# Kernel tuning notes

Hardware: AMD Instinct MI355X
Metric: run time of the kernel (lower is better)

Reference implementation:

```python
import jax, jax.numpy as jnp
import numpy as np

SAMPLE_SIZE = 8192
K = 8
N_SPLATS = 1_000_000
EPS = 1e-12  # keeps sqrt grad finite on zero-distance (duplicate) pairs


def setup_inputs() -> dict:
    key = jax.random.key(0)
    k1, k2, k3 = jax.random.split(key, 3)
    means = jax.random.normal(k1, (N_SPLATS, 3), dtype=jnp.float32)
    sh0 = jax.random.normal(k2, (N_SPLATS, 1, 3), dtype=jnp.float32)
    idx = jax.random.randint(k3, (SAMPLE_SIZE,), 0, N_SPLATS, dtype=jnp.int64)
    return {"means": means, "sh0": sh0, "idx": idx}


def reference(means, sh0, idx):
    sh0 = sh0.squeeze(1)                    # [N, 3]
    sm = means[idx]                         # [S, 3] sampled positions
    ss = sh0[idx]                           # [S, 3] sampled colors
    # pairwise euclidean distances (torch.cdist, p=2): [S, S]
    sq = jnp.sum(sm * sm, axis=-1)
    d2 = sq[:, None] + sq[None, :] - 2.0 * (sm @ sm.T)
    dist = jnp.sqrt(jnp.maximum(d2, EPS))
    # k+1 smallest per row; drop self (column 0)
    _, knn_idx = jax.lax.top_k(-dist, K + 1)           # [S, K+1]
    knn_idx = knn_idx[:, 1:]                           # [S, K]
    neighbors_sh0 = ss[knn_idx]                        # [S, K, 3]
    neighbor_dist = jnp.take_along_axis(dist, knn_idx, axis=1)[..., None]  # [S, K, 1]
    weight = jnp.exp(-neighbor_dist)
    diff = ss[:, None, :] - neighbors_sh0              # [S, K, 3]
    return jnp.mean(weight * diff * diff)
```

## Files before the change

### kernel.cpp

```cpp
#include <hip/hip_runtime.h>
#include <float.h>
#include <math.h>

#define NSAMPLE 8192
#define KSEL 9
#define KNN 8
#define BLK 512
#define EPS_F 1e-12f

#define ROWS_PB 8
#define NBLOCKS (NSAMPLE / ROWS_PB)
#define RPT 8
#define LANES 64
#define KQT 16
#define CHUNK 128
#define NCHUNK (1024 / CHUNK)
#define BNDI 4
#define WCAP 28
#define BP 129
#define IDX_MASK 0x1FFFu
#define VAL_MASK 0xFFFFE000u
#define PROW 73
#define SROW 145
#define SCALE (1.0f / (float)(NSAMPLE * KNN * 3))

#define SMEM_BYTES 40256
#define OFF_SCRATCH 4128
#define OFF_PARTS   8768
#define OFF_WL      32768
#define OFF_WCNT    39936
#define OFF_BND     40192
#define OFF_RED     40224

__device__ __forceinline__ unsigned umn(unsigned a, unsigned b) { return a < b ? a : b; }
__device__ __forceinline__ unsigned umx(unsigned a, unsigned b) { return a > b ? a : b; }

__device__ __forceinline__ void insert9(unsigned s[KSEL], unsigned x)
{
#pragma unroll
    for (int k = 0; k < KSEL - 1; ++k)
        s[k] = umx(s[k + 1], umn(x, s[k]));
    s[KSEL - 1] = umn(x, s[KSEL - 1]);
}

__device__ __forceinline__ unsigned pack_d2(float d2, int gidx)
{
    return (__float_as_uint(fmaxf(d2, 0.0f)) & VAL_MASK) | (unsigned)gidx;
}

__device__ __forceinline__ float sfl(float x)
{
    return __uint_as_float((unsigned)__builtin_amdgcn_readfirstlane(
        (int)__float_as_uint(x)));
}

__device__ __forceinline__ unsigned mbcnt64(unsigned long long m)
{
    return __builtin_amdgcn_mbcnt_hi((unsigned)(m >> 32),
           __builtin_amdgcn_mbcnt_lo((unsigned)(m & 0xFFFFFFFFull), 0u));
}

__device__ __forceinline__ void load_lds16(const float4* g, float4* l)
{
    __builtin_amdgcn_global_load_lds(
        (const __attribute__((address_space(1))) void*)g,
        (__attribute__((address_space(3))) void*)l, 16, 0, 0);
}

__global__ __launch_bounds__(256) void gather_k(
    const float* __restrict__ means, const float* __restrict__ sh0,
    const int* __restrict__ idx,
    float4* __restrict__ sm4, float4* __restrict__ ss4)
{
    int i = blockIdx.x * 256 + threadIdx.x;
    if (i >= NSAMPLE) return;
    int id = idx[i];
    const float* m = means + 3 * id;
    const float* s = sh0 + 3 * id;
    float mx = m[0], my = m[1], mz = m[2];
    sm4[i] = make_float4(mx, my, mz, fmaf(mx, mx, fmaf(my, my, mz * mz)));
    ss4[i] = make_float4(s[0], s[1], s[2], 0.0f);
}

#define QUAD(R, Q, CI)                                                        \
    {                                                                         \
        float v0 = fmaf(cX[(R) + 0], (Q).x, fmaf(cY[(R) + 0], (Q).y,          \
                   fmaf(cZ[(R) + 0], (Q).z, (Q).w)));                         \
        float v1 = fmaf(cX[(R) + 1], (Q).x, fmaf(cY[(R) + 1], (Q).y,          \
                   fmaf(cZ[(R) + 1], (Q).z, (Q).w)));                         \
        float v2 = fmaf(cX[(R) + 2], (Q).x, fmaf(cY[(R) + 2], (Q).y,          \
                   fmaf(cZ[(R) + 2], (Q).z, (Q).w)));                         \
        float v3 = fmaf(cX[(R) + 3], (Q).x, fmaf(cY[(R) + 3], (Q).y,          \
                   fmaf(cZ[(R) + 3], (Q).z, (Q).w)));                         \
        unsigned long long m0 = __ballot(v0 <= sb[(R) + 0]);                  \
        unsigned long long m1 = __ballot(v1 <= sb[(R) + 1]);                  \
        unsigned long long m2 = __ballot(v2 <= sb[(R) + 2]);                  \
        unsigned long long m3 = __ballot(v3 <= sb[(R) + 3]);                  \
        if (m0) {                                                             \
            unsigned pos = base[(R) + 0] + mbcnt64(m0);                       \
            if ((v0 <= sb[(R) + 0]) && pos < WCAP)                            \
                wl[(w * RPT + (R) + 0) * WCAP + pos] =                        \
                    pack_d2(v0 + cW[(R) + 0], (CI));                          \
            base[(R) + 0] += (unsigned)__popcll(m0);                          \
        }                                                                     \
        if (m1) {                                                             \
            unsigned pos = base[(R) + 1] + mbcnt64(m1);                       \
            if ((v1 <= sb[(R) + 1]) && pos < WCAP)                            \
                wl[(w * RPT + (R) + 1) * WCAP + pos] =                        \
                    pack_d2(v1 + cW[(R) + 1], (CI));                          \
            base[(R) + 1] += (unsigned)__popcll(m1);                          \
        }                                                                     \
        if (m2) {                                                             \
            unsigned pos = base[(R) + 2] + mbcnt64(m2);                       \
            if ((v2 <= sb[(R) + 2]) && pos < WCAP)                            \
                wl[(w * RPT + (R) + 2) * WCAP + pos] =                        \
                    pack_d2(v2 + cW[(R) + 2], (CI));                          \
            base[(R) + 2] += (unsigned)__popcll(m2);                          \
        }                                                                     \
        if (m3) {                                                             \
            unsigned pos = base[(R) + 3] + mbcnt64(m3);                       \
            if ((v3 <= sb[(R) + 3]) && pos < WCAP)                            \
                wl[(w * RPT + (R) + 3) * WCAP + pos] =                        \
                    pack_d2(v3 + cW[(R) + 3], (CI));                          \
            base[(R) + 3] += (unsigned)__popcll(m3);                          \
        }                                                                     \
    }

__global__ __launch_bounds__(BLK, 8) void main_k(
    const float4* __restrict__ sm4, const float4* __restrict__ ss4,
    float* __restrict__ partial)
{
    __shared__ __align__(16) unsigned char smem[SMEM_BYTES];
    float4*   stg     = (float4*)smem;
    unsigned* bpart   = (unsigned*)smem;
    unsigned* scratch = (unsigned*)(smem + OFF_SCRATCH);
    unsigned* partS   = (unsigned*)(smem + OFF_PARTS);
    unsigned* wl      = (unsigned*)(smem + OFF_WL);
    unsigned* wcnt    = (unsigned*)(smem + OFF_WCNT);
    unsigned* bnd     = (unsigned*)(smem + OFF_BND);
    float*    red     = (float*)(smem + OFF_RED);

    const int t = threadIdx.x;
    const int lane = t & (LANES - 1);
    const int w = t >> 6;

    float cX[RPT], cY[RPT], cZ[RPT], cW[RPT];
#pragma unroll
    for (int i = 0; i < RPT; ++i) {
        float4 p = sm4[blockIdx.x * ROWS_PB + i];
        cX[i] = sfl(-2.0f * p.x);
        cY[i] = sfl(-2.0f * p.y);
        cZ[i] = sfl(-2.0f * p.z);
        cW[i] = sfl(p.w);
    }

    {
        unsigned pm[RPT];
#pragma unroll
        for (int i = 0; i < RPT; ++i) pm[i] = 0xFFFFFFFFu;
        const int b0 = w * (KQT * LANES);
        const float4* __restrict__ bp = sm4 + b0 + lane;
#pragma unroll
        for (int k = 0; k < BNDI; ++k) {
            const int ci = b0 + k * LANES + lane;
            float4 q = bp[k * LANES];
#pragma unroll
            for (int i = 0; i < RPT; ++i) {
                float s = fmaf(cX[i], q.x,
                          fmaf(cY[i], q.y, fmaf(cZ[i], q.z, q.w)));
                pm[i] = umn(pm[i], pack_d2(s + cW[i], ci));
            }
        }
#pragma unroll
        for (int i = 0; i < RPT; ++i) {
            pm[i] = umn(pm[i], (unsigned)__shfl_xor((int)pm[i], 32, 64));
            pm[i] = umn(pm[i], (unsigned)__shfl_xor((int)pm[i], 16, 64));
        }
        if (lane < 16) {
#pragma unroll
            for (int i = 0; i < RPT; ++i)
                bpart[i * BP + w * 16 + lane] = pm[i];
        }
    }
    __syncthreads();

    if (t < 128) {
        const int r1 = t & (ROWS_PB - 1);
        const int g = t >> 3;
        unsigned s[KSEL];
#pragma unroll
        for (int k = 0; k < KSEL; ++k) s[k] = 0xFFFFFFFFu;
#pragma unroll
        for (int e = 0; e < 8; ++e)
            insert9(s, bpart[r1 * BP + g * 8 + e]);
#pragma unroll
        for (int k = 0; k < KSEL; ++k)
            scratch[r1 * SROW + g * KSEL + k] = s[k];
    }
    __syncthreads();
    if (t < 64) {
        const int r1 = t & (ROWS_PB - 1);
        const int mg = t >> 3;
        unsigned m[KSEL];
#pragma unroll
        for (int k = 0; k < KSEL; ++k) m[k] = 0xFFFFFFFFu;
#pragma unroll
        for (int e = 0; e < 2 * KSEL; ++e)
            insert9(m, scratch[r1 * SROW + (2 * mg) * KSEL + e]);
#pragma unroll
        for (int k = 0; k < KSEL; ++k)
            partS[r1 * PROW + mg * KSEL + k] = m[k];
    }
    __syncthreads();
    if (t < ROWS_PB) {
        unsigned m[KSEL];
#pragma unroll
        for (int k = 0; k < KSEL; ++k) m[k] = 0xFFFFFFFFu;
#pragma unroll
        for (int e = 0; e < 8 * KSEL; ++e)
            insert9(m, partS[t * PROW + e]);
        bnd[t] = m[0];
    }
    __syncthreads();

    float sb[RPT];
#pragma unroll
    for (int i = 0; i < RPT; ++i) {
        float bfv = __uint_as_float(bnd[i] | IDX_MASK);
        float D = bfv - cW[i];
        sb[i] = sfl(D + (bfv + fabsf(D)) * 6.0e-7f + 1e-33f);
    }

    unsigned base[RPT];
#pragma unroll
    for (int i = 0; i < RPT; ++i) base[i] = 0u;

    const int s0 = w * (KQT * LANES);
    const float4* __restrict__ gsrc = sm4 + s0;

    load_lds16(gsrc + lane,      stg + (w * 2 + 0) * CHUNK);
    load_lds16(gsrc + 64 + lane, stg + (w * 2 + 0) * CHUNK + 64);

#pragma unroll 1
    for (int c = 0; c < NCHUNK; ++c) {
        const float4* gn = gsrc + (c + 1) * CHUNK;
        float4* ln = stg + (w * 2 + ((c + 1) & 1)) * CHUNK;
        load_lds16(gn + lane,      ln);
        load_lds16(gn + 64 + lane, ln + 64);

        asm volatile("s_waitcnt vmcnt(2)" ::: "memory");
        __builtin_amdgcn_sched_barrier(0);

        const float4* buf = stg + (w * 2 + (c & 1)) * CHUNK;
        float4 q0 = buf[lane];
        float4 q1 = buf[64 + lane];
        const int ci0 = s0 + c * CHUNK + lane;
        QUAD(0, q0, ci0)
        QUAD(4, q0, ci0)
        QUAD(0, q1, ci0 + 64)
        QUAD(4, q1, ci0 + 64)
    }

    if (lane == 0) {
#pragma unroll
        for (int i = 0; i < RPT; ++i)
            wcnt[w * RPT + i] = umn(base[i], WCAP);
    }
    __syncthreads();

    if (t < 64) {
        const int r1 = t & (ROWS_PB - 1);
        const int wv = t >> 3;
        const int li = wv * RPT + r1;
        const unsigned n = wcnt[li];
        unsigned s[KSEL];
#pragma unroll
        for (int k = 0; k < KSEL; ++k) s[k] = 0xFFFFFFFFu;
        for (unsigned k = 0; k < n; ++k)
            insert9(s, wl[li * WCAP + k]);
#pragma unroll
        for (int k = 0; k < KSEL; ++k)
            partS[r1 * PROW + wv * KSEL + k] = s[k];
    }
    __syncthreads();

    if (t < ROWS_PB) {
        unsigned m[KSEL];
#pragma unroll
        for (int k = 0; k < KSEL; ++k) m[k] = 0xFFFFFFFFu;
#pragma unroll
        for (int e = 0; e < 8 * KSEL; ++e)
            insert9(m, partS[t * PROW + e]);

        const int gr = blockIdx.x * ROWS_PB + t;
        float4 pm4 = sm4[gr];
        float4 ps4 = ss4[gr];
        float acc = 0.0f;
#pragma unroll
        for (int k = 0; k < KNN; ++k) {
            int j = (int)(m[k] & IDX_MASK);
            float4 qm = sm4[j];
            float dx = pm4.x - qm.x, dy = pm4.y - qm.y, dz = pm4.z - qm.z;
            float d2 = fmaf(dx, dx, fmaf(dy, dy, dz * dz));
            float d = sqrtf(fmaxf(d2, EPS_F));
            float wgt = expf(-d);
            float4 qs = ss4[j];
            float ax = ps4.x - qs.x, ay = ps4.y - qs.y, az = ps4.z - qs.z;
            acc += wgt * (ax * ax + ay * ay + az * az);
        }
        red[t] = acc;
    }
    __syncthreads();
    if (t == 0) {
        float ssum = 0.0f;
#pragma unroll
        for (int i = 0; i < ROWS_PB; ++i) ssum += red[i];
        partial[blockIdx.x] = ssum;
    }
}

__global__ __launch_bounds__(256) void reduce_k(
    const float* __restrict__ partial, float* __restrict__ out)
{
    __shared__ float sbuf[4];
    int t = threadIdx.x;
    float v = 0.0f;
    for (int i = t; i < NBLOCKS; i += 256) v += partial[i];
    for (int off = 32; off > 0; off >>= 1) v += __shfl_down(v, off);
    if ((t & 63) == 0) sbuf[t >> 6] = v;
    __syncthreads();
    if (t == 0) {
        float s = sbuf[0] + sbuf[1] + sbuf[2] + sbuf[3];
        out[0] = s * SCALE;
    }
}

extern "C" void kernel_launch(void* const* d_in, const int* in_sizes, int n_in,
                              void* d_out, int out_size, void* d_ws, size_t ws_size,
                              hipStream_t stream)
{
    const float* means = (const float*)d_in[0];
    const float* sh0   = (const float*)d_in[1];
    const int*   idxp  = (const int*)d_in[2];

    float4* sm4 = (float4*)d_ws;
    float4* ss4 = sm4 + NSAMPLE;
    float*  partial = (float*)(ss4 + NSAMPLE);

    gather_k<<<NSAMPLE / 256, 256, 0, stream>>>(means, sh0, idxp, sm4, ss4);
    main_k<<<NBLOCKS, BLK, 0, stream>>>(sm4, ss4, partial);
    reduce_k<<<1, 256, 0, stream>>>(partial, (float*)d_out);
}
```

Baseline: 99.24 us.

## Replace serial top-9 merge trees with wave-parallel radix select and rank-based selection

The multi-stage serial insert9 merge trees, which ran on a few threads with extra barriers, are removed. The first bound is now found by a per-wave bitwise binary search using ballot and popcount over 128 packed candidates. The final top-8 selection is done by having each lane compute the rank of its candidate against all 72 partial results, then scattering the per-neighbor loss terms into a small shared array. This cuts serialized single-thread work and several __syncthreads, at the cost of redundant comparisons. It also relies on the packed keys being unique so that ranks are well defined.

```diff
diff --git a/kernel.cpp b/kernel.cpp
--- a/kernel.cpp
+++ b/kernel.cpp
@@ -17,20 +17,17 @@
 #define NCHUNK (1024 / CHUNK)
 #define BNDI 4
 #define WCAP 28
-#define BP 129
 #define IDX_MASK 0x1FFFu
 #define VAL_MASK 0xFFFFE000u
-#define PROW 73
-#define SROW 145
+#define PSEL 76
 #define SCALE (1.0f / (float)(NSAMPLE * KNN * 3))
 
-#define SMEM_BYTES 40256
-#define OFF_SCRATCH 4128
-#define OFF_PARTS   8768
 #define OFF_WL      32768
-#define OFF_WCNT    39936
-#define OFF_BND     40192
-#define OFF_RED     40224
+#define OFF_WCNT    (OFF_WL + 64 * WCAP * 4)
+#define OFF_BND     (OFF_WCNT + 256)
+#define OFF_RED     (OFF_BND + 32)
+#define OFF_TARR    (OFF_RED + 32)
+#define SMEM_BYTES  (OFF_TARR + 256)
 
 __device__ __forceinline__ unsigned umn(unsigned a, unsigned b) { return a < b ? a : b; }
 __device__ __forceinline__ unsigned umx(unsigned a, unsigned b) { return a > b ? a : b; }
@@ -131,14 +128,14 @@
     float* __restrict__ partial)
 {
     __shared__ __align__(16) unsigned char smem[SMEM_BYTES];
-    float4*   stg     = (float4*)smem;
-    unsigned* bpart   = (unsigned*)smem;
-    unsigned* scratch = (unsigned*)(smem + OFF_SCRATCH);
-    unsigned* partS   = (unsigned*)(smem + OFF_PARTS);
-    unsigned* wl      = (unsigned*)(smem + OFF_WL);
-    unsigned* wcnt    = (unsigned*)(smem + OFF_WCNT);
-    unsigned* bnd     = (unsigned*)(smem + OFF_BND);
-    float*    red     = (float*)(smem + OFF_RED);
+    float4*   stg   = (float4*)smem;
+    unsigned* bpart = (unsigned*)smem;
+    unsigned* partS = (unsigned*)smem;
+    unsigned* wl    = (unsigned*)(smem + OFF_WL);
+    unsigned* wcnt  = (unsigned*)(smem + OFF_WCNT);
+    unsigned* bnd   = (unsigned*)(smem + OFF_BND);
+    float*    red   = (float*)(smem + OFF_RED);
+    float*    tarr  = (float*)(smem + OFF_TARR);
 
     const int t = threadIdx.x;
     const int lane = t & (LANES - 1);
@@ -179,47 +176,23 @@
         if (lane < 16) {
 #pragma unroll
             for (int i = 0; i < RPT; ++i)
-                bpart[i * BP + w * 16 + lane] = pm[i];
-        }
-    }
-    __syncthreads();
-
-    if (t < 128) {
-        const int r1 = t & (ROWS_PB - 1);
-        const int g = t >> 3;
-        unsigned s[KSEL];
-#pragma unroll
-        for (int k = 0; k < KSEL; ++k) s[k] = 0xFFFFFFFFu;
-#pragma unroll
-        for (int e = 0; e < 8; ++e)
-            insert9(s, bpart[r1 * BP + g * 8 + e]);
-#pragma unroll
-        for (int k = 0; k < KSEL; ++k)
-            scratch[r1 * SROW + g * KSEL + k] = s[k];
-    }
-    __syncthreads();
-    if (t < 64) {
-        const int r1 = t & (ROWS_PB - 1);
-        const int mg = t >> 3;
-        unsigned m[KSEL];
-#pragma unroll
-        for (int k = 0; k < KSEL; ++k) m[k] = 0xFFFFFFFFu;
-#pragma unroll
-        for (int e = 0; e < 2 * KSEL; ++e)
-            insert9(m, scratch[r1 * SROW + (2 * mg) * KSEL + e]);
-#pragma unroll
-        for (int k = 0; k < KSEL; ++k)
-            partS[r1 * PROW + mg * KSEL + k] = m[k];
-    }
-    __syncthreads();
-    if (t < ROWS_PB) {
-        unsigned m[KSEL];
-#pragma unroll
-        for (int k = 0; k < KSEL; ++k) m[k] = 0xFFFFFFFFu;
-#pragma unroll
-        for (int e = 0; e < 8 * KSEL; ++e)
-            insert9(m, partS[t * PROW + e]);
-        bnd[t] = m[0];
+                bpart[i * 128 + w * 16 + lane] = pm[i];
+        }
+    }
+    __syncthreads();
+
+    {
+        const unsigned p0 = bpart[w * 128 + lane] >> 13;
+        const unsigned p1 = bpart[w * 128 + 64 + lane] >> 13;
+        unsigned P = 0;
+#pragma unroll 1
+        for (int b = 18; b >= 0; --b) {
+            const unsigned x = P + (1u << b) - 1u;
+            const unsigned cnt = (unsigned)__popcll(__ballot(p0 <= x))
+                               + (unsigned)__popcll(__ballot(p1 <= x));
+            if (cnt < 9u) P |= (1u << b);
+        }
+        if (lane == 0) bnd[w] = (P << 13);
     }
     __syncthreads();
 
@@ -280,25 +253,30 @@
             insert9(s, wl[li * WCAP + k]);
 #pragma unroll
         for (int k = 0; k < KSEL; ++k)
-            partS[r1 * PROW + wv * KSEL + k] = s[k];
-    }
-    __syncthreads();
-
-    if (t < ROWS_PB) {
-        unsigned m[KSEL];
-#pragma unroll
-        for (int k = 0; k < KSEL; ++k) m[k] = 0xFFFFFFFFu;
-#pragma unroll
-        for (int e = 0; e < 8 * KSEL; ++e)
-            insert9(m, partS[t * PROW + e]);
-
-        const int gr = blockIdx.x * ROWS_PB + t;
-        float4 pm4 = sm4[gr];
-        float4 ps4 = ss4[gr];
-        float acc = 0.0f;
-#pragma unroll
-        for (int k = 0; k < KNN; ++k) {
-            int j = (int)(m[k] & IDX_MASK);
+            partS[r1 * PSEL + wv * KSEL + k] = s[k];
+    }
+    if (t < 64) tarr[t] = 0.0f;
+    __syncthreads();
+
+    {
+        const int r1 = w;
+        const unsigned vA = partS[r1 * PSEL + lane];
+        const unsigned vB = (lane < 8) ? partS[r1 * PSEL + 64 + lane]
+                                       : 0xFFFFFFFFu;
+        unsigned rkA = 0, rkB = 0;
+#pragma unroll
+        for (int e = 0; e < 18; ++e) {
+            const uint4 u = *(const uint4*)&partS[r1 * PSEL + e * 4];
+            rkA += (unsigned)(u.x < vA) + (unsigned)(u.y < vA)
+                 + (unsigned)(u.z < vA) + (unsigned)(u.w < vA);
+            rkB += (unsigned)(u.x < vB) + (unsigned)(u.y < vB)
+                 + (unsigned)(u.z < vB) + (unsigned)(u.w < vB);
+        }
+        const int gr = blockIdx.x * ROWS_PB + r1;
+        if (rkA >= 1u && rkA <= 8u) {
+            const int j = (int)(vA & IDX_MASK);
+            float4 pm4 = sm4[gr];
+            float4 ps4 = ss4[gr];
             float4 qm = sm4[j];
             float dx = pm4.x - qm.x, dy = pm4.y - qm.y, dz = pm4.z - qm.z;
             float d2 = fmaf(dx, dx, fmaf(dy, dy, dz * dz));
@@ -306,8 +284,28 @@
             float wgt = expf(-d);
             float4 qs = ss4[j];
             float ax = ps4.x - qs.x, ay = ps4.y - qs.y, az = ps4.z - qs.z;
-            acc += wgt * (ax * ax + ay * ay + az * az);
-        }
+            tarr[r1 * 8 + (int)(rkA - 1u)] = wgt * (ax * ax + ay * ay + az * az);
+        }
+        if (lane < 8 && rkB >= 1u && rkB <= 8u) {
+            const int j = (int)(vB & IDX_MASK);
+            float4 pm4 = sm4[gr];
+            float4 ps4 = ss4[gr];
+            float4 qm = sm4[j];
+            float dx = pm4.x - qm.x, dy = pm4.y - qm.y, dz = pm4.z - qm.z;
+            float d2 = fmaf(dx, dx, fmaf(dy, dy, dz * dz));
+            float d = sqrtf(fmaxf(d2, EPS_F));
+            float wgt = expf(-d);
+            float4 qs = ss4[j];
+            float ax = ps4.x - qs.x, ay = ps4.y - qs.y, az = ps4.z - qs.z;
+            tarr[r1 * 8 + (int)(rkB - 1u)] = wgt * (ax * ax + ay * ay + az * az);
+        }
+    }
+    __syncthreads();
+
+    if (t < ROWS_PB) {
+        float acc = 0.0f;
+#pragma unroll
+        for (int k = 7; k >= 0; --k) acc += tarr[t * 8 + k];
         red[t] = acc;
     }
     __syncthreads();
```

Result: slower. 112.5 us (+13.3%).
